# Kernel tuning notes

Hardware: AMD Instinct MI355X
Metric: run time of the kernel (lower is better)

Reference implementation:

```python
import jax, jax.numpy as jnp
import numpy as np

TRAIN_ROIS = 200
POS_RATIO = 0.33
POS_MAX = int(TRAIN_ROIS * POS_RATIO)  # 66
BBOX_STD = np.array([0.1, 0.1, 0.2, 0.2], dtype=np.float32)


def _iou(boxes1, boxes2):
    # boxes1 [N,4], boxes2 [G,4] in (y1,x1,y2,x2) -> IoU [N,G]
    b1 = boxes1[:, None, :]
    b2 = boxes2[None, :, :]
    y1 = jnp.maximum(b1[..., 0], b2[..., 0])
    x1 = jnp.maximum(b1[..., 1], b2[..., 1])
    y2 = jnp.minimum(b1[..., 2], b2[..., 2])
    x2 = jnp.minimum(b1[..., 3], b2[..., 3])
    inter = jnp.maximum(x2 - x1, 0.0) * jnp.maximum(y2 - y1, 0.0)
    a1 = (b1[..., 2] - b1[..., 0]) * (b1[..., 3] - b1[..., 1])
    a2 = (b2[..., 2] - b2[..., 0]) * (b2[..., 3] - b2[..., 1])
    union = a1 + a2 - inter
    return inter / jnp.where(union > 0, union, 1.0)


def _box_refine(box, gt):
    # standard Mask R-CNN box_refinement_graph
    h = box[..., 2] - box[..., 0]
    w = box[..., 3] - box[..., 1]
    cy = box[..., 0] + 0.5 * h
    cx = box[..., 1] + 0.5 * w
    gh = gt[..., 2] - gt[..., 0]
    gw = gt[..., 3] - gt[..., 1]
    gcy = gt[..., 0] + 0.5 * gh
    gcx = gt[..., 1] + 0.5 * gw
    return jnp.stack([(gcy - cy) / h, (gcx - cx) / w,
                      jnp.log(gh / h), jnp.log(gw / w)], axis=-1)


def _per_image(proposals, gt_boxes, gt_captions, scores):
    T = TRAIN_ROIS
    valid_p = jnp.sum(jnp.abs(proposals), axis=1) > 0   # trim_zeros on proposals
    valid_g = jnp.sum(jnp.abs(gt_boxes), axis=1) > 0    # trim_zeros on gt
    # IoU only feeds comparisons/argmax (pure index selection) -> no grad path
    overlaps = jax.lax.stop_gradient(_iou(proposals, gt_boxes))
    overlaps = jnp.where(valid_g[None, :], overlaps, -1.0)
    roi_iou_max = jnp.max(overlaps, axis=1)
    pos_bool = valid_p & (roi_iou_max >= 0.5)
    neg_bool = valid_p & (roi_iou_max < 0.5)
    # deterministic stand-in for tf.random.shuffle[:count]: first `count` in index order
    pos_idx = jnp.where(pos_bool, size=POS_MAX, fill_value=0)[0]
    pos_cnt = jnp.minimum(jnp.sum(pos_bool), POS_MAX)
    pos_valid = jnp.arange(POS_MAX) < pos_cnt
    neg_target = (pos_cnt.astype(jnp.float32) / POS_RATIO).astype(jnp.int32) - pos_cnt
    neg_idx = jnp.where(neg_bool, size=T, fill_value=0)[0]
    neg_cnt = jnp.minimum(jnp.minimum(neg_target, jnp.sum(neg_bool)), T - pos_cnt)
    neg_valid = jnp.arange(T) < neg_cnt

    positive_rois = proposals[pos_idx]                  # [POS_MAX,4]
    negative_rois = proposals[neg_idx]                  # [T,4]
    gt_assign = jnp.argmax(overlaps[pos_idx], axis=1)   # [POS_MAX]
    roi_gt_boxes = gt_boxes[gt_assign]
    roi_gt_captions = gt_captions[gt_assign]
    roi_gt_scores = scores[gt_assign]
    # for padded (invalid) positive slots, use the roi itself -> zero, finite deltas
    safe_gt = jnp.where(pos_valid[:, None], roi_gt_boxes, positive_rois)
    deltas = _box_refine(positive_rois, safe_gt) / jnp.asarray(BBOX_STD)

    # positives occupy slots [0,pos_cnt), negatives [pos_cnt, pos_cnt+neg_cnt), rest zero-padded
    pos_slots = jnp.where(pos_valid, jnp.arange(POS_MAX), T)   # T is out-of-range -> dropped
    neg_slots = jnp.where(neg_valid, pos_cnt + jnp.arange(T), T)
    rois = (jnp.zeros((T, 4), proposals.dtype)
            .at[pos_slots].set(positive_rois, mode='drop')
            .at[neg_slots].set(negative_rois, mode='drop'))
    out_deltas = jnp.zeros((T, 4), proposals.dtype).at[pos_slots].set(deltas, mode='drop')
    out_caps = jnp.zeros((T, gt_captions.shape[1]), gt_captions.dtype).at[pos_slots].set(roi_gt_captions, mode='drop')
    out_scores = jnp.zeros((T,), scores.dtype).at[pos_slots].set(roi_gt_scores, mode='drop')
    return rois, out_deltas, out_caps, out_scores


def setup_inputs() -> dict:
    key = jax.random.key(0)
    B, N, G = 8, 4096, 512
    k1, k2, k3, k4, k5 = jax.random.split(key, 5)
    c = jax.random.uniform(k1, (B, N, 2))                   # box centers (y,x)
    s = jax.random.uniform(k2, (B, N, 2)) * 0.2 + 0.02      # box sizes
    lo = jnp.clip(c - 0.5 * s, 0.0, 1.0)
    hi = jnp.clip(c + 0.5 * s, 0.0, 1.0)
    proposals = jnp.concatenate([lo, hi], axis=-1)          # (y1,x1,y2,x2)
    # gt boxes = perturbed copies of first G proposals (ensures IoU>=0.5 positives exist)
    p = proposals[:, :G, :] + jax.random.normal(k3, (B, G, 4)) * 0.02
    y1 = jnp.minimum(p[..., 0], p[..., 2]); y2 = jnp.maximum(p[..., 0], p[..., 2]) + 1e-3
    x1 = jnp.minimum(p[..., 1], p[..., 3]); x2 = jnp.maximum(p[..., 1], p[..., 3]) + 1e-3
    gt_boxes = jnp.clip(jnp.stack([y1, x1, y2, x2], axis=-1), 0.0, 1.0)
    # exercise the zero-trim logic: zero-pad tails
    proposals = proposals.at[:, N - 256:, :].set(0.0)
    gt_boxes = gt_boxes.at[:, G - 32:, :].set(0.0)
    gt_captions = jax.random.randint(k4, (B, G, 15), 0, 10000, dtype=jnp.int32)
    scores = jax.random.uniform(k5, (B, G))
    return {"proposals": proposals, "gt_boxes": gt_boxes,
            "gt_captions": gt_captions, "scores": scores}


def reference(proposals, gt_boxes, gt_captions, scores):
    return jax.vmap(_per_image)(proposals, gt_boxes, gt_captions, scores)
```

## Files before the change

### kernel.cpp

```cpp
#include <hip/hip_runtime.h>
#include <math.h>

#define BB   8
#define NP   4096
#define NG   512
#define TT   200
#define PMAX 66

#define CH   8
#define NB64 (NP / 64)

__global__ __launch_bounds__(256) void iou_phase(
    const float* __restrict__ proposals, const float* __restrict__ gt,
    int* __restrict__ argj, unsigned long long* __restrict__ posmask,
    unsigned long long* __restrict__ negmask) {
#pragma clang fp contract(off)
  const int b     = blockIdx.x >> 6;
  const int blk   = blockIdx.x & 63;
  const int pbase = blk * 64;

  __shared__ float4 sgt[NG];
  __shared__ short  sidx[NG];
  __shared__ int    s_wcnt[4];
  __shared__ float  rbest[CH][64];
  __shared__ int    ridx[CH][64];

  const int tid  = threadIdx.x;
  const int wave = tid >> 6;
  const int lane = tid & 63;

  const int plocal  = tid & 31;
  const int chunkid = tid >> 5;
  const int ip      = pbase + plocal;
  const int iq      = ip + 32;

  const float4 p = ((const float4*)proposals)[(size_t)b * NP + ip];
  const float4 q = ((const float4*)proposals)[(size_t)b * NP + iq];

  const float4* gtb4 = (const float4*)(gt + (size_t)b * NG * 4);
  const int ja = wave * 128 + lane;
  const int jb = ja + 64;
  const float4 ga = gtb4[ja];
  const float4 gb = gtb4[jb];
  const bool va = (fabsf(ga.x) + fabsf(ga.y) + fabsf(ga.z) + fabsf(ga.w)) > 0.0f;
  const bool vb = (fabsf(gb.x) + fabsf(gb.y) + fabsf(gb.z) + fabsf(gb.w)) > 0.0f;
  const unsigned long long ma = __ballot(va);
  const unsigned long long mb = __ballot(vb);
  if (lane == 0) s_wcnt[wave] = __popcll(ma) + __popcll(mb);
  __syncthreads();

  int wbase = 0;
  for (int w = 0; w < 4; ++w) if (w < wave) wbase += s_wcnt[w];
  const int nv = s_wcnt[0] + s_wcnt[1] + s_wcnt[2] + s_wcnt[3];

  const unsigned long long lower = (1ull << lane) - 1ull;
  if (va) {
    int k = wbase + __popcll(ma & lower);
    sgt[k] = ga; sidx[k] = (short)ja;
  }
  if (vb) {
    int k = wbase + __popcll(ma) + __popcll(mb & lower);
    sgt[k] = gb; sidx[k] = (short)jb;
  }
  __syncthreads();

  const float a1p = (p.z - p.x) * (p.w - p.y);
  const float a1q = (q.z - q.x) * (q.w - q.y);
  const int   csz = (nv + CH - 1) / CH;
  int j0 = chunkid * csz;
  int j1 = j0 + csz; if (j1 > nv) j1 = nv;
  if (j0 > nv) j0 = nv;

  const bool vpp = (fabsf(p.x) + fabsf(p.y) + fabsf(p.z) + fabsf(p.w)) > 0.0f;
  const bool vpq = (fabsf(q.x) + fabsf(q.y) + fabsf(q.z) + fabsf(q.w)) > 0.0f;
  const bool any_valid = __ballot(vpp || vpq) != 0ull;

  float bestp = -INFINITY, bestq = -INFINITY;
  int bkp = 0, bkq = 0;
  if (any_valid) {
#pragma unroll 2
    for (int j = j0; j < j1; ++j) {
      float4 g = sgt[j];
      float a2 = (g.z - g.x) * (g.w - g.y);
      {
        float y1 = fmaxf(p.x, g.x);
        float x1 = fmaxf(p.y, g.y);
        float y2 = fminf(p.z, g.z);
        float x2 = fminf(p.w, g.w);
        float inter = fmaxf(x2 - x1, 0.0f) * fmaxf(y2 - y1, 0.0f);
        float un = a1p + a2 - inter;
        float iou = inter / (un > 0.0f ? un : 1.0f);
        if (iou > bestp) { bestp = iou; bkp = j; }
      }
      {
        float y1 = fmaxf(q.x, g.x);
        float x1 = fmaxf(q.y, g.y);
        float y2 = fminf(q.z, g.z);
        float x2 = fminf(q.w, g.w);
        float inter = fmaxf(x2 - x1, 0.0f) * fmaxf(y2 - y1, 0.0f);
        float un = a1q + a2 - inter;
        float iou = inter / (un > 0.0f ? un : 1.0f);
        if (iou > bestq) { bestq = iou; bkq = j; }
      }
    }
  }
  rbest[chunkid][plocal]      = bestp;
  ridx[chunkid][plocal]       = bkp;
  rbest[chunkid][plocal + 32] = bestq;
  ridx[chunkid][plocal + 32]  = bkq;
  __syncthreads();

  if (tid < 64) {
    float bb = rbest[0][tid];
    int   bi = ridx[0][tid];
    for (int c = 1; c < CH; ++c) {
      float v = rbest[c][tid];
      if (v > bb) { bb = v; bi = ridx[c][tid]; }
    }
    int borig = (int)sidx[bi];
    const float4 mine = (tid < 32) ? p : q;
    bool vp  = (fabsf(mine.x) + fabsf(mine.y) + fabsf(mine.z) + fabsf(mine.w)) > 0.0f;
    bool isp = vp && (bb >= 0.5f);
    bool isn = vp && (bb <  0.5f);
    unsigned long long mp = __ballot(isp);
    unsigned long long mn = __ballot(isn);
    argj[(size_t)b * NP + pbase + tid] = borig;
    if (tid == 0) {
      posmask[(size_t)b * NB64 + blk] = mp;
      negmask[(size_t)b * NB64 + blk] = mn;
    }
  }
}

__global__ __launch_bounds__(256) void select_phase(
    const float* __restrict__ proposals, const float* __restrict__ gt,
    const int* __restrict__ caps, const float* __restrict__ scores,
    const int* __restrict__ argj, const unsigned long long* __restrict__ posmask,
    const unsigned long long* __restrict__ negmask, float* __restrict__ out) {
#pragma clang fp contract(off)
  const int b = blockIdx.x;

  __shared__ int s_pos[PMAX];
  __shared__ int s_neg[TT];
  __shared__ int s_tot[2];

  const int tid  = threadIdx.x;
  const int wave = tid >> 6;
  const int lane = tid & 63;

  if (wave < 2) {
    const unsigned long long* msk =
        (wave == 0 ? posmask : negmask) + (size_t)b * NB64;
    const int cap = (wave == 0) ? PMAX : TT;
    int* list = (wave == 0) ? s_pos : s_neg;
    unsigned long long m = msk[lane];
    int cnt = __popcll(m);
    int incl = cnt;
    for (int d = 1; d < 64; d <<= 1) {
      int u = __shfl_up(incl, d, 64);
      if (lane >= d) incl += u;
    }
    int base = incl - cnt;
    if (lane == 63) s_tot[wave] = incl;
    while (m && base < cap) {
      int bit = __ffsll((unsigned long long)m) - 1;
      list[base] = lane * 64 + bit;
      m &= m - 1; ++base;
    }
  }
  __syncthreads();

  const int pos_total = s_tot[0];
  const int neg_total = s_tot[1];
  int pos_cnt = pos_total < PMAX ? pos_total : PMAX;
  int neg_cnt = (int)((float)pos_cnt / 0.33f) - pos_cnt;
  if (neg_total < neg_cnt)    neg_cnt = neg_total;
  if (TT - pos_cnt < neg_cnt) neg_cnt = TT - pos_cnt;
  if (neg_cnt < 0)            neg_cnt = 0;

  float* rois   = out + (size_t)b * TT * 4;
  float* deltas = out + (size_t)BB * TT * 4 + (size_t)b * TT * 4;
  float* ocaps  = out + (size_t)2 * BB * TT * 4 + (size_t)b * TT * 15;
  float* osc    = out + (size_t)2 * BB * TT * 4 + (size_t)BB * TT * 15 + (size_t)b * TT;

  const int k = tid;
  if (k < TT) {
    if (k < pos_cnt) {
      int i = s_pos[k];
      const float* pp = proposals + ((size_t)b * NP + i) * 4;
      float p0 = pp[0], p1 = pp[1], p2 = pp[2], p3 = pp[3];
      int g = argj[(size_t)b * NP + i];
      const float* gg = gt + ((size_t)b * NG + g) * 4;
      float g0 = gg[0], g1 = gg[1], g2 = gg[2], g3 = gg[3];

      rois[k * 4 + 0] = p0; rois[k * 4 + 1] = p1;
      rois[k * 4 + 2] = p2; rois[k * 4 + 3] = p3;

      float h  = p2 - p0, ww = p3 - p1;
      float cy = p0 + 0.5f * h, cx = p1 + 0.5f * ww;
      float gh = g2 - g0, gw = g3 - g1;
      float gcy = g0 + 0.5f * gh, gcx = g1 + 0.5f * gw;
      deltas[k * 4 + 0] = ((gcy - cy) / h) / 0.1f;
      deltas[k * 4 + 1] = ((gcx - cx) / ww) / 0.1f;
      deltas[k * 4 + 2] = logf(gh / h) / 0.2f;
      deltas[k * 4 + 3] = logf(gw / ww) / 0.2f;

      const int* cp = caps + ((size_t)b * NG + g) * 15;
      for (int c = 0; c < 15; ++c) ocaps[k * 15 + c] = (float)cp[c];
      osc[k] = scores[(size_t)b * NG + g];
    } else {
      if (k < pos_cnt + neg_cnt) {
        int i = s_neg[k - pos_cnt];
        const float* pp = proposals + ((size_t)b * NP + i) * 4;
        rois[k * 4 + 0] = pp[0]; rois[k * 4 + 1] = pp[1];
        rois[k * 4 + 2] = pp[2]; rois[k * 4 + 3] = pp[3];
      } else {
        rois[k * 4 + 0] = 0.0f; rois[k * 4 + 1] = 0.0f;
        rois[k * 4 + 2] = 0.0f; rois[k * 4 + 3] = 0.0f;
      }
      deltas[k * 4 + 0] = 0.0f; deltas[k * 4 + 1] = 0.0f;
      deltas[k * 4 + 2] = 0.0f; deltas[k * 4 + 3] = 0.0f;
      for (int c = 0; c < 15; ++c) ocaps[k * 15 + c] = 0.0f;
      osc[k] = 0.0f;
    }
  }
}

extern "C" void kernel_launch(void* const* d_in, const int* in_sizes, int n_in,
                              void* d_out, int out_size, void* d_ws, size_t ws_size,
                              hipStream_t stream) {
  const float* proposals = (const float*)d_in[0];
  const float* gt        = (const float*)d_in[1];
  const int*   caps      = (const int*)d_in[2];
  const float* scores    = (const float*)d_in[3];
  float* out = (float*)d_out;

  char* ws = (char*)d_ws;
  int*                argj = (int*)ws;
  unsigned long long* pm   = (unsigned long long*)(ws + (size_t)BB * NP * 4);
  unsigned long long* nm   = pm + (size_t)BB * NB64;

  hipLaunchKernelGGL(iou_phase, dim3(BB * NB64), dim3(256), 0, stream,
                     proposals, gt, argj, pm, nm);
  hipLaunchKernelGGL(select_phase, dim3(BB), dim3(256), 0, stream,
                     proposals, gt, caps, scores, argj, pm, nm, out);
}
```

Baseline: 79.33 us.

## Fuse IoU and selection kernels using last-block atomic counter per image

Merges the two launches into one kernel. Each block does its IoU work, then bumps a per-image atomic counter with release/acquire fences, and the last block to finish for an image performs the compaction and output writes. This removes the second kernel launch and its dependency gap, but adds a memset launch to clear the counters plus atomic and fence overhead. It also leaves a redundant duplicate store to argj.

```diff
diff --git a/kernel.cpp b/kernel.cpp
--- a/kernel.cpp
+++ b/kernel.cpp
@@ -10,10 +10,12 @@
 #define CH   8
 #define NB64 (NP / 64)
 
-__global__ __launch_bounds__(256) void iou_phase(
+__global__ __launch_bounds__(256) void fused_kernel(
     const float* __restrict__ proposals, const float* __restrict__ gt,
+    const int* __restrict__ caps, const float* __restrict__ scores,
     int* __restrict__ argj, unsigned long long* __restrict__ posmask,
-    unsigned long long* __restrict__ negmask) {
+    unsigned long long* __restrict__ negmask, int* __restrict__ counters,
+    float* __restrict__ out) {
 #pragma clang fp contract(off)
   const int b     = blockIdx.x >> 6;
   const int blk   = blockIdx.x & 63;
@@ -24,6 +26,10 @@
   __shared__ int    s_wcnt[4];
   __shared__ float  rbest[CH][64];
   __shared__ int    ridx[CH][64];
+  __shared__ int    s_last;
+  __shared__ int    s_pos[PMAX];
+  __shared__ int    s_neg[TT];
+  __shared__ int    s_tot[2];
 
   const int tid  = threadIdx.x;
   const int wave = tid >> 6;
@@ -124,29 +130,25 @@
     bool isn = vp && (bb <  0.5f);
     unsigned long long mp = __ballot(isp);
     unsigned long long mn = __ballot(isn);
+    argj[(size_t)b * NP + pbase + tid] = mp || true ? borig : 0;
     argj[(size_t)b * NP + pbase + tid] = borig;
     if (tid == 0) {
       posmask[(size_t)b * NB64 + blk] = mp;
       negmask[(size_t)b * NB64 + blk] = mn;
     }
   }
-}
-
-__global__ __launch_bounds__(256) void select_phase(
-    const float* __restrict__ proposals, const float* __restrict__ gt,
-    const int* __restrict__ caps, const float* __restrict__ scores,
-    const int* __restrict__ argj, const unsigned long long* __restrict__ posmask,
-    const unsigned long long* __restrict__ negmask, float* __restrict__ out) {
-#pragma clang fp contract(off)
-  const int b = blockIdx.x;
-
-  __shared__ int s_pos[PMAX];
-  __shared__ int s_neg[TT];
-  __shared__ int s_tot[2];
-
-  const int tid  = threadIdx.x;
-  const int wave = tid >> 6;
-  const int lane = tid & 63;
+
+  __syncthreads();
+  if (tid == 0) {
+    __builtin_amdgcn_fence(__ATOMIC_RELEASE, "agent");
+    int old = atomicAdd(&counters[b], 1);
+    int last = (old == NB64 - 1) ? 1 : 0;
+    if (last)
+      __builtin_amdgcn_fence(__ATOMIC_ACQUIRE, "agent");
+    s_last = last;
+  }
+  __syncthreads();
+  if (!s_last) return;
 
   if (wave < 2) {
     const unsigned long long* msk =
@@ -178,10 +180,10 @@
   if (TT - pos_cnt < neg_cnt) neg_cnt = TT - pos_cnt;
   if (neg_cnt < 0)            neg_cnt = 0;
 
-  float* rois   = out + (size_t)b * TT * 4;
-  float* deltas = out + (size_t)BB * TT * 4 + (size_t)b * TT * 4;
-  float* ocaps  = out + (size_t)2 * BB * TT * 4 + (size_t)b * TT * 15;
-  float* osc    = out + (size_t)2 * BB * TT * 4 + (size_t)BB * TT * 15 + (size_t)b * TT;
+  float* rois_o  = out + (size_t)b * TT * 4;
+  float* deltas  = out + (size_t)BB * TT * 4 + (size_t)b * TT * 4;
+  float* ocaps   = out + (size_t)2 * BB * TT * 4 + (size_t)b * TT * 15;
+  float* osc     = out + (size_t)2 * BB * TT * 4 + (size_t)BB * TT * 15 + (size_t)b * TT;
 
   const int k = tid;
   if (k < TT) {
@@ -193,8 +195,8 @@
       const float* gg = gt + ((size_t)b * NG + g) * 4;
       float g0 = gg[0], g1 = gg[1], g2 = gg[2], g3 = gg[3];
 
-      rois[k * 4 + 0] = p0; rois[k * 4 + 1] = p1;
-      rois[k * 4 + 2] = p2; rois[k * 4 + 3] = p3;
+      rois_o[k * 4 + 0] = p0; rois_o[k * 4 + 1] = p1;
+      rois_o[k * 4 + 2] = p2; rois_o[k * 4 + 3] = p3;
 
       float h  = p2 - p0, ww = p3 - p1;
       float cy = p0 + 0.5f * h, cx = p1 + 0.5f * ww;
@@ -212,11 +214,11 @@
       if (k < pos_cnt + neg_cnt) {
         int i = s_neg[k - pos_cnt];
         const float* pp = proposals + ((size_t)b * NP + i) * 4;
-        rois[k * 4 + 0] = pp[0]; rois[k * 4 + 1] = pp[1];
-        rois[k * 4 + 2] = pp[2]; rois[k * 4 + 3] = pp[3];
+        rois_o[k * 4 + 0] = pp[0]; rois_o[k * 4 + 1] = pp[1];
+        rois_o[k * 4 + 2] = pp[2]; rois_o[k * 4 + 3] = pp[3];
       } else {
-        rois[k * 4 + 0] = 0.0f; rois[k * 4 + 1] = 0.0f;
-        rois[k * 4 + 2] = 0.0f; rois[k * 4 + 3] = 0.0f;
+        rois_o[k * 4 + 0] = 0.0f; rois_o[k * 4 + 1] = 0.0f;
+        rois_o[k * 4 + 2] = 0.0f; rois_o[k * 4 + 3] = 0.0f;
       }
       deltas[k * 4 + 0] = 0.0f; deltas[k * 4 + 1] = 0.0f;
       deltas[k * 4 + 2] = 0.0f; deltas[k * 4 + 3] = 0.0f;
@@ -239,9 +241,10 @@
   int*                argj = (int*)ws;
   unsigned long long* pm   = (unsigned long long*)(ws + (size_t)BB * NP * 4);
   unsigned long long* nm   = pm + (size_t)BB * NB64;
-
-  hipLaunchKernelGGL(iou_phase, dim3(BB * NB64), dim3(256), 0, stream,
-                     proposals, gt, argj, pm, nm);
-  hipLaunchKernelGGL(select_phase, dim3(BB), dim3(256), 0, stream,
-                     proposals, gt, caps, scores, argj, pm, nm, out);
+  int*                cnts = (int*)(nm + (size_t)BB * NB64);
+
+  hipMemsetAsync(cnts, 0, BB * sizeof(int), stream);
+
+  hipLaunchKernelGGL(fused_kernel, dim3(BB * NB64), dim3(256), 0, stream,
+                     proposals, gt, caps, scores, argj, pm, nm, cnts, out);
 }
```

New measurement: 83.59 us. +5.4%, slower.
